# Performance work log

Measured on AMD Instinct MI355X. Metric: run time of the kernel, lower is better.

Reference implementation:

```python
import jax, jax.numpy as jnp
import numpy as np

B, S, E, H, FF = 4, 2048, 512, 8, 2048
DH = E // H
EPS = 1e-6


def setup_inputs() -> dict:
    key = jax.random.key(0)
    ks = jax.random.split(key, 16)
    sc = lambda fan_in: 1.0 / np.sqrt(fan_in)
    inp = {
        "x": jax.random.normal(ks[0], (B, S, E), dtype=jnp.float32),
        "src_mask": jnp.ones((B, 1, 1, S), dtype=jnp.int32),
        # attention projections, stored [in, out]
        "wq": jax.random.uniform(ks[1], (E, E), minval=-sc(E), maxval=sc(E)),
        "bq": jnp.zeros((E,), jnp.float32),
        "wk": jax.random.uniform(ks[2], (E, E), minval=-sc(E), maxval=sc(E)),
        "bk": jnp.zeros((E,), jnp.float32),
        "wv": jax.random.uniform(ks[3], (E, E), minval=-sc(E), maxval=sc(E)),
        "bv": jnp.zeros((E,), jnp.float32),
        "wo": jax.random.uniform(ks[4], (E, E), minval=-sc(E), maxval=sc(E)),
        "bo": jnp.zeros((E,), jnp.float32),
        # feed-forward
        "w1": jax.random.uniform(ks[5], (E, FF), minval=-sc(E), maxval=sc(E)),
        "b1": jnp.zeros((FF,), jnp.float32),
        "w2": jax.random.uniform(ks[6], (FF, E), minval=-sc(FF), maxval=sc(FF)),
        "b2": jnp.zeros((E,), jnp.float32),
        # addNormLayer scalar params (alpha init 1, bias init 0)
        "alpha1": jnp.ones((1,), jnp.float32),
        "beta1": jnp.zeros((1,), jnp.float32),
        "alpha2": jnp.ones((1,), jnp.float32),
        "beta2": jnp.zeros((1,), jnp.float32),
    }
    return inp


def _norm(x, alpha, beta):
    # matches torch: mean + unbiased std (ddof=1), eps added to std
    mean = jnp.mean(x, axis=-1, keepdims=True)
    std = jnp.std(x, axis=-1, keepdims=True, ddof=1)
    return alpha * (x - mean) / (std + EPS) + beta


def reference(x, src_mask, wq, bq, wk, bk, wv, bv, wo, bo,
              w1, b1, w2, b2, alpha1, beta1, alpha2, beta2):
    # --- residual 1: pre-norm self-attention ---
    n = _norm(x, alpha1, beta1)  # [B,S,E]
    q = (n @ wq + bq).reshape(B, S, H, DH).transpose(0, 2, 1, 3)  # [B,H,S,DH]
    k = (n @ wk + bk).reshape(B, S, H, DH).transpose(0, 2, 1, 3)
    v = (n @ wv + bv).reshape(B, S, H, DH).transpose(0, 2, 1, 3)
    scores = jnp.einsum('bhqd,bhkd->bhqk', q, k) / np.sqrt(DH)  # [B,H,S,S]
    scores = jnp.where(src_mask == 0, -1e9, scores)
    attn = jax.nn.softmax(scores, axis=-1)
    ctx = jnp.einsum('bhqk,bhkd->bhqd', attn, v)  # [B,H,S,DH]
    ctx = ctx.transpose(0, 2, 1, 3).reshape(B, S, E)
    x = x + (ctx @ wo + bo)
    # --- residual 2: pre-norm FFN ---
    n2 = _norm(x, alpha2, beta2)
    ff = jax.nn.relu(n2 @ w1 + b1) @ w2 + b2
    return x + ff
```

## Files before the change

kernel.cpp:

```cpp
#include <hip/hip_runtime.h>

typedef __bf16 bfrag __attribute__((ext_vector_type(8)));
typedef float f32x4 __attribute__((ext_vector_type(4)));
typedef float f32x16 __attribute__((ext_vector_type(16)));
typedef unsigned short us8 __attribute__((ext_vector_type(8)));
typedef unsigned int u32x2 __attribute__((ext_vector_type(2)));
typedef unsigned int u32x4 __attribute__((ext_vector_type(4)));

__device__ __forceinline__ float bf2f(unsigned short s) {
  unsigned u = ((unsigned)s) << 16;
  float f;
  __builtin_memcpy(&f, &u, 4);
  return f;
}
__device__ __forceinline__ unsigned short f2bf(float f) {
  unsigned u;
  __builtin_memcpy(&u, &f, 4);
  u += 0x7fffu + ((u >> 16) & 1u);
  return (unsigned short)(u >> 16);
}
__device__ __forceinline__ float rdf(const void* p, size_t i, int isf) {
  return isf ? ((const float*)p)[i] : bf2f(((const unsigned short*)p)[i]);
}
__device__ __forceinline__ void gld16(const unsigned short* g, unsigned short* l) {
  __builtin_amdgcn_global_load_lds(
      (const __attribute__((address_space(1))) unsigned int*)g,
      (__attribute__((address_space(3))) unsigned int*)l, 16, 0, 0);
}
__device__ __forceinline__ unsigned cvtpk_bf16(float a, float b) {
  unsigned d;
  asm("v_cvt_pk_bf16_f32 %0, %1, %2" : "=v"(d) : "v"(a), "v"(b));
  return d;
}

template <int XMODE>
__device__ void norm_unit(const void* xin, const void* alpha, const void* beta,
                          unsigned short* out, int isf, int u) {
  constexpr int E = 512;
  int xf = XMODE ? 1 : isf;
  int tid = threadIdx.x;
  int wave = tid >> 6, lane = tid & 63;
  size_t tok = (size_t)u * 4 + wave;
  float v[8];
  if (xf) {
    const float* xp = (const float*)xin + tok * E + lane * 8;
    float4 a0 = *(const float4*)xp;
    float4 a1 = *(const float4*)(xp + 4);
    v[0] = a0.x; v[1] = a0.y; v[2] = a0.z; v[3] = a0.w;
    v[4] = a1.x; v[5] = a1.y; v[6] = a1.z; v[7] = a1.w;
  } else {
    us8 uu = *(const us8*)((const unsigned short*)xin + tok * E + lane * 8);
#pragma unroll
    for (int j = 0; j < 8; j++) v[j] = bf2f(uu[j]);
  }
  float s = 0.f, sq = 0.f;
#pragma unroll
  for (int j = 0; j < 8; j++) { s += v[j]; sq += v[j] * v[j]; }
#pragma unroll
  for (int off = 1; off < 64; off <<= 1) {
    s += __shfl_xor(s, off, 64);
    sq += __shfl_xor(sq, off, 64);
  }
  float mean = s * (1.0f / 512.0f);
  float var = fmaxf((sq - 512.0f * mean * mean) * (1.0f / 511.0f), 0.0f);
  float inv = rdf(alpha, 0, isf) / (sqrtf(var) + 1e-6f);
  float be = rdf(beta, 0, isf);
  us8 ov;
#pragma unroll
  for (int j = 0; j < 8; j++) ov[j] = f2bf((v[j] - mean) * inv + be);
  *(us8*)(out + tok * E + lane * 8) = ov;
}

__global__ __launch_bounds__(256) void setup_k(
    const unsigned short* __restrict__ x16,
    const void* wq, const void* wk, const void* wv, const void* wo,
    const void* w1, const void* w2,
    unsigned short* wqkvT, unsigned short* woT,
    unsigned short* w1T, unsigned short* w2T,
    const void* bq, const void* bk, const void* bv, const void* bo,
    const void* b1, const void* b2, float* __restrict__ bcat,
    const void* alpha1, const void* beta1, unsigned short* __restrict__ n1,
    int* __restrict__ flag) {
  __shared__ unsigned short tile[32][33];
  __shared__ int s_cnt;
  int tid = threadIdx.x;
  int bid = blockIdx.x;
  if (tid == 0) s_cnt = 0;
  __syncthreads();
  {
    int c = 0;
    for (int i = tid; i < 4096; i += 256) {
      unsigned short s = x16[2 * i];
      int e = (s >> 7) & 0xFF;
      if (e > 0xC2 || (e != 0 && e < 0x3D)) c++;
    }
    atomicAdd(&s_cnt, c);
  }
  __syncthreads();
  const int isf = (s_cnt > 256) ? 1 : 0;
  if (bid == 0 && tid == 0) flag[0] = isf;

  if (bid >= 3090) {
    norm_unit<0>(x16, alpha1, beta1, n1, isf, bid - 3090);
    return;
  }
  if (bid >= 3072) {
    int i = (bid - 3072) * 256 + tid;
    if (i < 4608) {
      float v;
      if (i < 512) v = rdf(bq, i, isf);
      else if (i < 1024) v = rdf(bk, i - 512, isf);
      else if (i < 1536) v = rdf(bv, i - 1024, isf);
      else if (i < 2048) v = rdf(bo, i - 1536, isf);
      else if (i < 4096) v = rdf(b1, i - 2048, isf);
      else v = rdf(b2, i - 4096, isf);
      bcat[i] = v;
    }
    return;
  }
  const void* W;
  unsigned short* Wt;
  int K, N, t;
  if (bid < 1024) {
    K = 512; N = 512; t = bid & 255;
    if (bid < 256) { W = wq; Wt = wqkvT; }
    else if (bid < 512) { W = wk; Wt = wqkvT + 262144; }
    else if (bid < 768) { W = wv; Wt = wqkvT + 524288; }
    else { W = wo; Wt = woT; }
  } else if (bid < 2048) {
    W = w1; Wt = w1T; K = 512; N = 2048; t = bid - 1024;
  } else {
    W = w2; Wt = w2T; K = 2048; N = 512; t = bid - 2048;
  }
  int nx = N >> 5;
  int n0 = (t % nx) * 32, k0 = (t / nx) * 32;
#pragma unroll
  for (int i = 0; i < 4; i++) {
    int e = tid + i * 256;
    int r = e >> 5, c = e & 31;
    tile[r][c] = f2bf(rdf(W, (size_t)(k0 + r) * N + n0 + c, isf));
  }
  __syncthreads();
#pragma unroll
  for (int i = 0; i < 4; i++) {
    int e = tid + i * 256;
    int r = e >> 5, c = e & 31;
    Wt[(size_t)(n0 + r) * K + k0 + c] = tile[c][r];
  }
}

__global__ __launch_bounds__(256) void vtrans_k(
    const unsigned short* __restrict__ qkb, unsigned short* __restrict__ vbt) {
  __shared__ unsigned short tile[32][33];
  int tid = threadIdx.x;
  int u = blockIdx.x;
  int s0 = (u & 63) * 32;
  int d0 = ((u >> 6) & 1) * 32;
  int bh = u >> 7, b = bh >> 3, h = bh & 7;
#pragma unroll
  for (int i = 0; i < 4; i++) {
    int e = tid + i * 256;
    int r = e >> 5, c = e & 31;
    tile[r][c] = qkb[((size_t)b * 2048 + s0 + r) * 1536 + 1024 + h * 64 + d0 + c];
  }
  __syncthreads();
#pragma unroll
  for (int i = 0; i < 4; i++) {
    int e = tid + i * 256;
    int r = e >> 5, c = e & 31;
    vbt[((size_t)bh * 64 + d0 + r) * 2048 + s0 + c] = tile[c][r];
  }
}

__global__ __launch_bounds__(256) void norm2_k(
    const void* __restrict__ xin, const void* __restrict__ alpha,
    const void* __restrict__ beta, unsigned short* __restrict__ out,
    const int* __restrict__ flag) {
  norm_unit<1>(xin, alpha, beta, out, flag[0], blockIdx.x);
}

template <int TN, int RES, int OUTM, int RELU>
__global__ __launch_bounds__(256, 3) void gemm2_k(
    const unsigned short* __restrict__ A,
    const unsigned short* __restrict__ Bt,
    const float* __restrict__ bias,
    const void* __restrict__ res,
    void* __restrict__ outp,
    int N, int K, const int* __restrict__ flag) {
  constexpr int MT = (TN == 128) ? 4 : 2;
  constexpr int BROWS = TN / 4;
  __shared__ alignas(16) unsigned short As[128 * 64];
  __shared__ alignas(16) unsigned short Bs[TN * 64];
  int isf = flag[0];
  int outf32 = (OUTM == 1) || (OUTM == 2 && isf);
  int tid = threadIdx.x;
  int wave = tid >> 6, lane = tid & 63;
  int quad = lane >> 4, l16 = lane & 15, l7 = l16 & 7;
  int wm = (TN == 128) ? (wave >> 1) : wave;
  int wn = (TN == 128) ? (wave & 1) : 0;
  size_t m0 = (size_t)blockIdx.x * 128;
  size_t n0 = (size_t)blockIdx.y * TN;

  int lrow = lane >> 3;
  int gcol = 8 * ((lane & 7) ^ lrow);

  const unsigned short* ag = A + (m0 + wave * 32 + lrow) * K + gcol;
  const unsigned short* bg = Bt + (n0 + wave * BROWS + lrow) * K + gcol;
  unsigned short* asl = &As[(wave * 32) * 64];
  unsigned short* bsl = &Bs[(wave * BROWS) * 64];

  f32x4 acc[MT][4];
#pragma unroll
  for (int i = 0; i < MT; i++)
#pragma unroll
    for (int j = 0; j < 4; j++) acc[i][j] = {0.f, 0.f, 0.f, 0.f};

  for (int k0 = 0; k0 < K; k0 += 64) {
    __syncthreads();
#pragma unroll
    for (int c = 0; c < 4; c++)
      gld16(ag + (size_t)(8 * c) * K + k0, asl + (8 * c) * 64);
#pragma unroll
    for (int c = 0; c < BROWS / 8; c++)
      gld16(bg + (size_t)(8 * c) * K + k0, bsl + (8 * c) * 64);
    __syncthreads();
#pragma unroll
    for (int ko = 0; ko < 2; ko++) {
      int slot = ((4 * ko + quad) ^ l7) * 8;
      bfrag af[MT], bf[4];
#pragma unroll
      for (int i = 0; i < MT; i++)
        af[i] = *(const bfrag*)&As[(wm * (MT * 16) + i * 16 + l16) * 64 + slot];
#pragma unroll
      for (int j = 0; j < 4; j++)
        bf[j] = *(const bfrag*)&Bs[(wn * 64 + j * 16 + l16) * 64 + slot];
#pragma unroll
      for (int i = 0; i < MT; i++)
#pragma unroll
        for (int j = 0; j < 4; j++)
          acc[i][j] = __builtin_amdgcn_mfma_f32_16x16x32_bf16(af[i], bf[j], acc[i][j], 0, 0, 0);
    }
  }
#pragma unroll
  for (int j = 0; j < 4; j++) {
    size_t n = n0 + wn * 64 + j * 16 + l16;
    float bv = bias[n];
#pragma unroll
    for (int i = 0; i < MT; i++) {
#pragma unroll
      for (int r = 0; r < 4; r++) {
        size_t m = m0 + wm * (MT * 16) + i * 16 + quad * 4 + r;
        float vv = acc[i][j][r] + bv;
        if (RELU) vv = fmaxf(vv, 0.0f);
        if (RES == 1) vv += rdf(res, m * N + n, isf);
        else if (RES == 2) vv += ((const float*)res)[m * N + n];
        if (outf32) ((float*)outp)[m * N + n] = vv;
        else ((unsigned short*)outp)[m * N + n] = f2bf(vv);
      }
    }
  }
}

__global__ __launch_bounds__(256, 2) void attn_k(
    const unsigned short* __restrict__ qkb,
    const unsigned short* __restrict__ vbt,
    const int* __restrict__ mask,
    unsigned short* __restrict__ ctx) {
  constexpr int S = 2048;
  __shared__ alignas(16) unsigned short Kt[2][64 * 64];
  __shared__ alignas(16) unsigned short Vt[2][64 * 64];
  __shared__ alignas(16) float mskf[S];
  __shared__ float linv[128];
  int tid = threadIdx.x, wave = tid >> 6, lane = tid & 63;
  int l32 = lane & 31, hi = lane >> 5;

  int lin = blockIdx.x;
  int work = (lin & 7) * 64 + (lin >> 3);
  int bh = work >> 4;
  int q0 = (work & 15) * 128;
  int b = bh >> 3, h = bh & 7;
  size_t rowbase = (size_t)b * S;
  const float SC = 0.18033688f;

  bfrag qf[4];
  {
    const unsigned short* qp =
        qkb + (rowbase + q0 + wave * 32 + l32) * 1536 + h * 64 + hi * 8;
#pragma unroll
    for (int ds = 0; ds < 4; ds++) qf[ds] = *(const bfrag*)(qp + ds * 16);
  }

  int srow_l = lane >> 3;
  int sc = lane & 7;
  const unsigned short* kgb = qkb + 512 + h * 64;
  const unsigned short* vgb = vbt + (size_t)bh * 64 * S;

  auto STAGE = [&](int buf, int kt) {
#pragma unroll
    for (int i = 0; i < 2; i++) {
      int r = wave * 16 + i * 8 + srow_l;
      gld16(kgb + (rowbase + kt + r) * 1536 + (size_t)((sc ^ (r & 7)) * 8),
            &Kt[buf][(wave * 16 + i * 8) * 64]);
      gld16(vgb + (size_t)r * S + kt + (size_t)((sc ^ (r & 7)) * 8),
            &Vt[buf][(wave * 16 + i * 8) * 64]);
    }
  };

  f32x16 o[2];
#pragma unroll
  for (int i = 0; i < 16; i++) { o[0][i] = 0.f; o[1][i] = 0.f; }
  float l_i = 0.f;

  STAGE(0, 0);
  for (int i = tid; i < S; i += 256) mskf[i] = mask[rowbase + i] ? 0.0f : -1e5f;
  __syncthreads();

  for (int it = 0; it < S / 64; it++) {
    int kt = it * 64;
    int cur = it & 1;
    if (it + 1 < S / 64) STAGE(cur ^ 1, kt + 64);

    f32x16 pacc[2];
#pragma unroll
    for (int t = 0; t < 2; t++)
#pragma unroll
      for (int i = 0; i < 16; i++) pacc[t][i] = 0.f;
#pragma unroll
    for (int t = 0; t < 2; t++) {
      int r = t * 32 + l32;
#pragma unroll
      for (int ds = 0; ds < 4; ds++) {
        int phys = ((2 * ds + hi) ^ (r & 7)) * 8;
        bfrag kf = *(const bfrag*)&Kt[cur][r * 64 + phys];
        pacc[t] = __builtin_amdgcn_mfma_f32_32x32x16_bf16(kf, qf[ds], pacc[t], 0, 0, 0);
      }
    }

    unsigned pb[2][8];
#pragma unroll
    for (int t = 0; t < 2; t++) {
#pragma unroll
      for (int g = 0; g < 4; g++) {
        float4 m4 = *(const float4*)&mskf[kt + t * 32 + g * 8 + hi * 4];
        float p0 = __builtin_amdgcn_exp2f(fminf(fmaf(pacc[t][g * 4 + 0], SC, m4.x), 50.0f));
        float p1 = __builtin_amdgcn_exp2f(fminf(fmaf(pacc[t][g * 4 + 1], SC, m4.y), 50.0f));
        float p2 = __builtin_amdgcn_exp2f(fminf(fmaf(pacc[t][g * 4 + 2], SC, m4.z), 50.0f));
        float p3 = __builtin_amdgcn_exp2f(fminf(fmaf(pacc[t][g * 4 + 3], SC, m4.w), 50.0f));
        l_i += (p0 + p1) + (p2 + p3);
        pb[t][g * 2] = cvtpk_bf16(p0, p1);
        pb[t][g * 2 + 1] = cvtpk_bf16(p2, p3);
      }
    }

#pragma unroll
    for (int ks = 0; ks < 4; ks++) {
      int t = ks >> 1, e = ks & 1;
      u32x2 sA = __builtin_amdgcn_permlane32_swap(pb[t][4 * e + 0], pb[t][4 * e + 2], false, false);
      u32x2 sB = __builtin_amdgcn_permlane32_swap(pb[t][4 * e + 1], pb[t][4 * e + 3], false, false);
      u32x4 pw = {sA.x, sB.x, sA.y, sB.y};
      bfrag pf = __builtin_bit_cast(bfrag, pw);
#pragma unroll
      for (int dt = 0; dt < 2; dt++) {
        int r = dt * 32 + l32;
        int phys = ((2 * ks + hi) ^ (r & 7)) * 8;
        bfrag vf = *(const bfrag*)&Vt[cur][r * 64 + phys];
        o[dt] = __builtin_amdgcn_mfma_f32_32x32x16_bf16(pf, vf, o[dt], 0, 0, 0);
      }
    }
    __syncthreads();
  }

  {
    unsigned lu = __builtin_bit_cast(unsigned, l_i);
    u32x2 lr = __builtin_amdgcn_permlane32_swap(lu, lu, false, false);
    float l_tot = __builtin_bit_cast(float, lr.x) + __builtin_bit_cast(float, lr.y);
    if (lane < 32) linv[wave * 32 + l32] = 1.0f / fmaxf(l_tot, 1e-30f);
  }
  __syncthreads();
#pragma unroll
  for (int dt = 0; dt < 2; dt++) {
#pragma unroll
    for (int reg = 0; reg < 16; reg++) {
      int ql = (reg & 3) + 8 * (reg >> 2) + 4 * hi;
      size_t qrow = rowbase + q0 + wave * 32 + ql;
      ctx[qrow * 512 + h * 64 + dt * 32 + l32] =
          f2bf(o[dt][reg] * linv[wave * 32 + ql]);
    }
  }
}

extern "C" void kernel_launch(void* const* d_in, const int* in_sizes, int n_in,
                              void* d_out, int out_size, void* d_ws, size_t ws_size,
                              hipStream_t stream) {
  const unsigned short* x = (const unsigned short*)d_in[0];
  const int* mask         = (const int*)d_in[1];
  const void* wq = d_in[2];  const void* bq = d_in[3];
  const void* wk = d_in[4];  const void* bk = d_in[5];
  const void* wv = d_in[6];  const void* bv = d_in[7];
  const void* wo = d_in[8];  const void* bo = d_in[9];
  const void* w1 = d_in[10]; const void* b1 = d_in[11];
  const void* w2 = d_in[12]; const void* b2 = d_in[13];
  const void* alpha1 = d_in[14]; const void* beta1 = d_in[15];
  const void* alpha2 = d_in[16]; const void* beta2 = d_in[17];

  char* ws = (char*)d_ws;
  int* flag            = (int*)(ws + 0);
  unsigned short* wqkvT= (unsigned short*)(ws + 65536);
  unsigned short* woT  = (unsigned short*)(ws + 1638400);
  unsigned short* w1T  = (unsigned short*)(ws + 2162688);
  unsigned short* w2T  = (unsigned short*)(ws + 4259840);
  float*          bcat = (float*)         (ws + 6356992);
  float*          x1   = (float*)         (ws + 6422528);
  unsigned short* n1   = (unsigned short*)(ws + 23199744);
  unsigned short* qkb  = (unsigned short*)(ws + 31588352);
  unsigned short* vbt  = (unsigned short*)(ws + 56754176);
  unsigned short* ff1  = qkb;

  dim3 blk(256);

  setup_k<<<5138, blk, 0, stream>>>(x, wq, wk, wv, wo, w1, w2,
                                    wqkvT, woT, w1T, w2T,
                                    bq, bk, bv, bo, b1, b2, bcat,
                                    alpha1, beta1, n1, flag);
  gemm2_k<128, 0, 0, 0><<<dim3(64, 12), blk, 0, stream>>>(n1, wqkvT, bcat, nullptr, qkb, 1536, 512, flag);
  vtrans_k<<<4096, blk, 0, stream>>>(qkb, vbt);
  attn_k<<<512, blk, 0, stream>>>(qkb, vbt, mask, n1);
  gemm2_k<64, 1, 1, 0><<<dim3(64, 8), blk, 0, stream>>>(n1, woT, bcat + 1536, (const void*)x, x1, 512, 512, flag);
  norm2_k<<<2048, blk, 0, stream>>>(x1, alpha2, beta2, n1, flag);
  gemm2_k<128, 0, 0, 1><<<dim3(64, 16), blk, 0, stream>>>(n1, w1T, bcat + 2048, nullptr, ff1, 2048, 512, flag);
  gemm2_k<64, 2, 2, 0><<<dim3(64, 8), blk, 0, stream>>>(ff1, w2T, bcat + 4096, x1, d_out, 512, 2048, flag);
}
```

Measured before the change: 284.7 us.

## Process two 64-key sub-tiles per iteration with interleaved QK/softmax/PV and setprio

The attention kernel now stages 128 keys per iteration as two 64-key halves. It interleaves the QK MFMAs of the second half with the softmax and PV of the first, using s_setprio to favour the MFMA phases. Global load pointers are precomputed and incremented instead of recomputed. The exp2 clamp is removed. Shared memory doubles, which may hurt occupancy, and the missing clamp risks overflow on large scores.

```diff
diff --git a/kernel.cpp b/kernel.cpp
--- a/kernel.cpp
+++ b/kernel.cpp
@@ -267,8 +267,8 @@
     const int* __restrict__ mask,
     unsigned short* __restrict__ ctx) {
   constexpr int S = 2048;
-  __shared__ alignas(16) unsigned short Kt[2][64 * 64];
-  __shared__ alignas(16) unsigned short Vt[2][64 * 64];
+  __shared__ alignas(16) unsigned short Kt[2][2][64 * 64];
+  __shared__ alignas(16) unsigned short Vt[2][2][64 * 64];
   __shared__ alignas(16) float mskf[S];
   __shared__ float linv[128];
   int tid = threadIdx.x, wave = tid >> 6, lane = tid & 63;
@@ -292,18 +292,31 @@
 
   int srow_l = lane >> 3;
   int sc = lane & 7;
+  int swz = (sc ^ srow_l) * 8;
   const unsigned short* kgb = qkb + 512 + h * 64;
   const unsigned short* vgb = vbt + (size_t)bh * 64 * S;
 
-  auto STAGE = [&](int buf, int kt) {
+  const unsigned short* kp[2][2];
+  const unsigned short* vp[2][2];
+#pragma unroll
+  for (int hh = 0; hh < 2; hh++)
 #pragma unroll
     for (int i = 0; i < 2; i++) {
       int r = wave * 16 + i * 8 + srow_l;
-      gld16(kgb + (rowbase + kt + r) * 1536 + (size_t)((sc ^ (r & 7)) * 8),
-            &Kt[buf][(wave * 16 + i * 8) * 64]);
-      gld16(vgb + (size_t)r * S + kt + (size_t)((sc ^ (r & 7)) * 8),
-            &Vt[buf][(wave * 16 + i * 8) * 64]);
-    }
+      kp[hh][i] = kgb + (rowbase + hh * 64 + r) * 1536 + swz;
+      vp[hh][i] = vgb + (size_t)r * S + hh * 64 + swz;
+    }
+
+  auto STAGE = [&](int buf) {
+#pragma unroll
+    for (int hh = 0; hh < 2; hh++)
+#pragma unroll
+      for (int i = 0; i < 2; i++) {
+        gld16(kp[hh][i], &Kt[buf][hh][(wave * 16 + i * 8) * 64]);
+        kp[hh][i] += 128 * 1536;
+        gld16(vp[hh][i], &Vt[buf][hh][(wave * 16 + i * 8) * 64]);
+        vp[hh][i] += 128;
+      }
   };
 
   f32x16 o[2];
@@ -311,62 +324,77 @@
   for (int i = 0; i < 16; i++) { o[0][i] = 0.f; o[1][i] = 0.f; }
   float l_i = 0.f;
 
-  STAGE(0, 0);
-  for (int i = tid; i < S; i += 256) mskf[i] = mask[rowbase + i] ? 0.0f : -1e5f;
-  __syncthreads();
-
-  for (int it = 0; it < S / 64; it++) {
-    int kt = it * 64;
-    int cur = it & 1;
-    if (it + 1 < S / 64) STAGE(cur ^ 1, kt + 64);
-
-    f32x16 pacc[2];
-#pragma unroll
-    for (int t = 0; t < 2; t++)
+  auto QK = [&](int hh, int cur, f32x16* pacc) {
+#pragma unroll
+    for (int t = 0; t < 2; t++) {
 #pragma unroll
       for (int i = 0; i < 16; i++) pacc[t][i] = 0.f;
-#pragma unroll
-    for (int t = 0; t < 2; t++) {
       int r = t * 32 + l32;
 #pragma unroll
       for (int ds = 0; ds < 4; ds++) {
-        int phys = ((2 * ds + hi) ^ (r & 7)) * 8;
-        bfrag kf = *(const bfrag*)&Kt[cur][r * 64 + phys];
+        int phys = ((2 * ds + hi) ^ (l32 & 7)) * 8;
+        bfrag kf = *(const bfrag*)&Kt[cur][hh][r * 64 + phys];
         pacc[t] = __builtin_amdgcn_mfma_f32_32x32x16_bf16(kf, qf[ds], pacc[t], 0, 0, 0);
       }
     }
-
-    unsigned pb[2][8];
+  };
+  auto SM = [&](int hh, int kt, const f32x16* pacc, unsigned* pb) {
 #pragma unroll
     for (int t = 0; t < 2; t++) {
 #pragma unroll
       for (int g = 0; g < 4; g++) {
-        float4 m4 = *(const float4*)&mskf[kt + t * 32 + g * 8 + hi * 4];
-        float p0 = __builtin_amdgcn_exp2f(fminf(fmaf(pacc[t][g * 4 + 0], SC, m4.x), 50.0f));
-        float p1 = __builtin_amdgcn_exp2f(fminf(fmaf(pacc[t][g * 4 + 1], SC, m4.y), 50.0f));
-        float p2 = __builtin_amdgcn_exp2f(fminf(fmaf(pacc[t][g * 4 + 2], SC, m4.z), 50.0f));
-        float p3 = __builtin_amdgcn_exp2f(fminf(fmaf(pacc[t][g * 4 + 3], SC, m4.w), 50.0f));
+        float4 m4 = *(const float4*)&mskf[kt + hh * 64 + t * 32 + g * 8 + hi * 4];
+        float p0 = __builtin_amdgcn_exp2f(fmaf(pacc[t][g * 4 + 0], SC, m4.x));
+        float p1 = __builtin_amdgcn_exp2f(fmaf(pacc[t][g * 4 + 1], SC, m4.y));
+        float p2 = __builtin_amdgcn_exp2f(fmaf(pacc[t][g * 4 + 2], SC, m4.z));
+        float p3 = __builtin_amdgcn_exp2f(fmaf(pacc[t][g * 4 + 3], SC, m4.w));
         l_i += (p0 + p1) + (p2 + p3);
-        pb[t][g * 2] = cvtpk_bf16(p0, p1);
-        pb[t][g * 2 + 1] = cvtpk_bf16(p2, p3);
+        pb[t * 8 + g * 2] = cvtpk_bf16(p0, p1);
+        pb[t * 8 + g * 2 + 1] = cvtpk_bf16(p2, p3);
       }
     }
-
+  };
+  auto PV = [&](int hh, int cur, const unsigned* pb) {
 #pragma unroll
     for (int ks = 0; ks < 4; ks++) {
       int t = ks >> 1, e = ks & 1;
-      u32x2 sA = __builtin_amdgcn_permlane32_swap(pb[t][4 * e + 0], pb[t][4 * e + 2], false, false);
-      u32x2 sB = __builtin_amdgcn_permlane32_swap(pb[t][4 * e + 1], pb[t][4 * e + 3], false, false);
+      u32x2 sA = __builtin_amdgcn_permlane32_swap(pb[t * 8 + 4 * e + 0], pb[t * 8 + 4 * e + 2], false, false);
+      u32x2 sB = __builtin_amdgcn_permlane32_swap(pb[t * 8 + 4 * e + 1], pb[t * 8 + 4 * e + 3], false, false);
       u32x4 pw = {sA.x, sB.x, sA.y, sB.y};
       bfrag pf = __builtin_bit_cast(bfrag, pw);
 #pragma unroll
       for (int dt = 0; dt < 2; dt++) {
         int r = dt * 32 + l32;
-        int phys = ((2 * ks + hi) ^ (r & 7)) * 8;
-        bfrag vf = *(const bfrag*)&Vt[cur][r * 64 + phys];
+        int phys = ((2 * ks + hi) ^ (l32 & 7)) * 8;
+        bfrag vf = *(const bfrag*)&Vt[cur][hh][r * 64 + phys];
         o[dt] = __builtin_amdgcn_mfma_f32_32x32x16_bf16(pf, vf, o[dt], 0, 0, 0);
       }
     }
+  };
+
+  STAGE(0);
+  for (int i = tid; i < S; i += 256) mskf[i] = mask[rowbase + i] ? 0.0f : -1e5f;
+  __syncthreads();
+
+  for (int it = 0; it < S / 128; it++) {
+    int kt = it * 128;
+    int cur = it & 1;
+    if (it + 1 < S / 128) STAGE(cur ^ 1);
+
+    f32x16 pacc0[2], pacc1[2];
+    unsigned pb0[16], pb1[16];
+    __builtin_amdgcn_s_setprio(1);
+    QK(0, cur, pacc0);
+    __builtin_amdgcn_s_setprio(0);
+    SM(0, kt, pacc0, pb0);
+    __builtin_amdgcn_s_setprio(1);
+    QK(1, cur, pacc1);
+    PV(0, cur, pb0);
+    __builtin_amdgcn_s_setprio(0);
+    SM(1, kt, pacc1, pb1);
+    __builtin_amdgcn_s_setprio(1);
+    PV(1, cur, pb1);
+    __builtin_amdgcn_s_setprio(0);
     __syncthreads();
   }
 
```

After: 276.6 us. 1.03x faster.
